# Kernel optimization log

Measured on AMD Instinct MI355X. Metric: run time of the kernel, lower is better.

## Reference

```python
import jax, jax.numpy as jnp
import numpy as np

B, L, D = 32, 128, 512
Qn = 16          # n_querys
N, P = 512, 64   # gathered groups x group size


def setup_inputs() -> dict:
    key = jax.random.key(0)
    ks = jax.random.split(key, 10)
    s = 0.02
    return {
        "patch": jax.random.normal(ks[0], (B, L, D), jnp.float32),
        "query": jax.random.normal(ks[1], (1, Qn, D), jnp.float32),
        "Wk": jax.random.normal(ks[2], (D, D), jnp.float32) * s,
        "bk": jnp.zeros((D,), jnp.float32),
        "Wv": jax.random.normal(ks[3], (D, D), jnp.float32) * s,
        "bv": jnp.zeros((D,), jnp.float32),
        "Wf": jax.random.normal(ks[4], (D, 1), jnp.float32) * s,
        "bf": jnp.zeros((1,), jnp.float32),
        "indices": jax.random.randint(ks[5], (N, P), 0, B * L),
        "pos_mask": jax.random.bernoulli(ks[6], 0.8, (N, P)),
    }


def reference(patch, query, Wk, bk, Wv, bv, Wf, bf, indices, pos_mask):
    # patch: [B,L,D]; query: [1,q,D]; indices: [N,P] into B*L; pos_mask: [N,P]
    b, l, d = patch.shape
    q = query.shape[1]
    scale = 1.0 / jnp.sqrt(jnp.asarray(d, patch.dtype))
    Q0 = query[0]                                   # [q,D]
    # Projections (proj_k/proj_v applied to [Q ; patch]); Q row identical across batch
    KQ = Q0 @ Wk + bk                               # [q,D]
    Kp = patch @ Wk + bk                            # [B,L,D]
    VQ = Q0 @ Wv + bv                               # [q,D]
    Vp = patch @ Wv + bv                            # [B,L,D]
    # attn scores: self-token column (same for every batch) + patch columns
    s_self = jnp.einsum('qd,qd->q', Q0, KQ) * scale            # [q]
    s_patch = jnp.einsum('qd,bld->blq', Q0, Kp) * scale        # [B,L,q]
    # gather groups of tokens by flat index
    g = s_patch.reshape(b * l, q)[indices]                     # [N,P,q]
    g = jnp.where(pos_mask[:, :, None], g, -jnp.inf)
    g = jnp.transpose(g, (0, 2, 1))                            # [N,q,P]
    scores = jnp.concatenate(
        [jnp.broadcast_to(s_self[None, :, None], (g.shape[0], q, 1)), g], axis=-1)
    w = jax.nn.softmax(scores, axis=-1)                        # [N,q,P+1]
    # gathered values (value of a token is independent of q in the original)
    Vg = Vp.reshape(b * l, d)[indices]                         # [N,P,D]
    Vg = jnp.where(pos_mask[:, :, None], Vg, 0.0)
    patch_token = w[:, :, 0:1] * VQ[None] \
        + jnp.einsum('nqp,npd->nqd', w[:, :, 1:], Vg)          # [N,q,D]
    # fusion attention pooling over the q query axis
    fw = jax.nn.softmax(jnp.einsum('nqd,do->nqo', patch_token, Wf) + bf, axis=1)
    return jnp.sum(patch_token * fw, axis=1)                   # [N,D]
```

## Files before the change

kernel.cpp:

```cpp
#include <hip/hip_runtime.h>
#include <hip/hip_bf16.h>
#include <math.h>

#define DD    512
#define QN    16
#define NTOK  4096
#define MEXT  4112
#define MPAD  4224
#define NGRP  512
#define PP    64
#define NB    640
#define SCALE 0.04419417382415922f

typedef __bf16 bf16x8 __attribute__((ext_vector_type(8)));
typedef float  f32x4  __attribute__((ext_vector_type(4)));

static __device__ __forceinline__ ushort f2bf(float f) {
    __hip_bfloat16 h = __float2bfloat16(f);
    return *reinterpret_cast<ushort*>(&h);
}
static __device__ __forceinline__ float2 bfp2f2(unsigned int v) {
    float2 r;
    r.x = __uint_as_float(v << 16);
    r.y = __uint_as_float(v & 0xffff0000u);
    return r;
}

__global__ __launch_bounds__(256) void pack_all(
    const float* __restrict__ patch, const float* __restrict__ query,
    const float* __restrict__ Wv, const float* __restrict__ Wk,
    const float* __restrict__ bk,
    ushort* __restrict__ Xb, ushort* __restrict__ Bb, float* __restrict__ c0)
{
    __shared__ float T[64][65];
    const int b = blockIdx.x;
    const int tid = threadIdx.x;
    if (b < 1056) {
        const int e0 = b * 2048 + tid * 8;
        const int row = e0 >> 9, c = e0 & 511;
        float v[8];
        if (row < NTOK) {
            const float4 a0 = *(const float4*)&patch[(size_t)row * DD + c];
            const float4 a1 = *(const float4*)&patch[(size_t)row * DD + c + 4];
            v[0]=a0.x; v[1]=a0.y; v[2]=a0.z; v[3]=a0.w;
            v[4]=a1.x; v[5]=a1.y; v[6]=a1.z; v[7]=a1.w;
        } else if (row < MEXT) {
            const float4 a0 = *(const float4*)&query[(size_t)(row - NTOK) * DD + c];
            const float4 a1 = *(const float4*)&query[(size_t)(row - NTOK) * DD + c + 4];
            v[0]=a0.x; v[1]=a0.y; v[2]=a0.z; v[3]=a0.w;
            v[4]=a1.x; v[5]=a1.y; v[6]=a1.z; v[7]=a1.w;
        } else {
#pragma unroll
            for (int j = 0; j < 8; ++j) v[j] = 0.f;
        }
        ushort o[8];
#pragma unroll
        for (int j = 0; j < 8; ++j) o[j] = f2bf(v[j]);
        *(uint4*)&Xb[e0] = *(const uint4*)o;
    } else if (b < 1120) {
        const int t = b - 1056;
        const int k0 = (t >> 3) * 64, n0 = (t & 7) * 64;
#pragma unroll
        for (int j = 0; j < 16; ++j) {
            const int idx = tid + j * 256;
            const int r = idx >> 6, c = idx & 63;
            T[r][c] = Wv[(size_t)(k0 + r) * DD + n0 + c];
        }
        __syncthreads();
#pragma unroll
        for (int j = 0; j < 16; ++j) {
            const int idx = tid + j * 256;
            const int r = idx >> 6, c = idx & 63;
            Bb[(size_t)(n0 + r) * DD + k0 + c] = f2bf(T[c][r]);
        }
    } else if (b < 1148) {
        const int e0 = (b - 1120) * 2048 + tid * 8;
        *(uint4*)&Bb[(size_t)528 * DD + e0] = make_uint4(0, 0, 0, 0);
    } else {
        const int wave = tid >> 6, lane = tid & 63;
        const int g = (b - 1148) * 4 + wave;
        if (g < DD) {
            const int e = g;
            float x[8];
#pragma unroll
            for (int j = 0; j < 8; ++j) x[j] = Wk[e * DD + j * 64 + lane];
            for (int q = 0; q < QN; ++q) {
                float s = 0.f;
#pragma unroll
                for (int j = 0; j < 8; ++j) s += x[j] * query[q * DD + j * 64 + lane];
#pragma unroll
                for (int off = 32; off > 0; off >>= 1) s += __shfl_down(s, off, 64);
                if (lane == 0) Bb[(size_t)(DD + q) * DD + e] = f2bf(s);
            }
        } else {
            const int q = g - DD;
            float s = 0.f;
#pragma unroll
            for (int j = 0; j < 8; ++j)
                s += bk[j * 64 + lane] * query[q * DD + j * 64 + lane];
#pragma unroll
            for (int off = 32; off > 0; off >>= 1) s += __shfl_down(s, off, 64);
            if (lane == 0) c0[q] = s;
        }
    }
}

__global__ __launch_bounds__(256) void k2_mfma(
    const ushort* __restrict__ Xb, const ushort* __restrict__ Bb,
    const float* __restrict__ bv, const float* __restrict__ c0,
    ushort* __restrict__ VpH, float* __restrict__ S)
{
    __shared__ __align__(16) ushort Xs[64][72];
    __shared__ __align__(16) ushort Bs[64][72];
    const int tid = threadIdx.x;
    const int rowBase = blockIdx.y * 64;
    const int colBase = blockIdx.x * 64;
    const int wave = tid >> 6, lane = tid & 63;
    const int wm = (wave >> 1) * 32, wn = (wave & 1) * 32;
    const int lr = lane & 15;
    const int quad = lane >> 4;

    f32x4 acc[2][2];
    const f32x4 zero = {0.f, 0.f, 0.f, 0.f};
#pragma unroll
    for (int i = 0; i < 2; ++i) { acc[i][0] = zero; acc[i][1] = zero; }

    for (int k0 = 0; k0 < DD; k0 += 64) {
#pragma unroll
        for (int i = 0; i < 2; ++i) {
            const int ch = tid + i * 256;
            const int r = ch >> 3, cc = (ch & 7) * 8;
            *(uint4*)&Xs[r][cc] = *(const uint4*)&Xb[(size_t)(rowBase + r) * DD + k0 + cc];
        }
#pragma unroll
        for (int i = 0; i < 2; ++i) {
            const int ch = tid + i * 256;
            const int r = ch >> 3, cc = (ch & 7) * 8;
            *(uint4*)&Bs[r][cc] = *(const uint4*)&Bb[(size_t)(colBase + r) * DD + k0 + cc];
        }
        __syncthreads();
#pragma unroll
        for (int kc = 0; kc < 2; ++kc) {
            bf16x8 af[2], bfr[2];
#pragma unroll
            for (int t = 0; t < 2; ++t)
                af[t] = *(const bf16x8*)&Xs[wm + t * 16 + lr][kc * 32 + quad * 8];
#pragma unroll
            for (int u = 0; u < 2; ++u)
                bfr[u] = *(const bf16x8*)&Bs[wn + u * 16 + lr][kc * 32 + quad * 8];
#pragma unroll
            for (int mt = 0; mt < 2; ++mt)
#pragma unroll
                for (int nt = 0; nt < 2; ++nt)
                    acc[mt][nt] = __builtin_amdgcn_mfma_f32_16x16x32_bf16(
                        af[mt], bfr[nt], acc[mt][nt], 0, 0, 0);
        }
        __syncthreads();
    }

#pragma unroll
    for (int nt = 0; nt < 2; ++nt) {
        const int col = colBase + wn + nt * 16 + lr;
        const bool isV = (col < DD);
        const bool isS = (col >= DD) && (col < DD + QN);
        const float badd = isV ? bv[col] : (isS ? c0[col - DD] : 0.f);
#pragma unroll
        for (int mt = 0; mt < 2; ++mt) {
#pragma unroll
            for (int r = 0; r < 4; ++r) {
                const int row = rowBase + wm + mt * 16 + quad * 4 + r;
                if (row < MEXT) {
                    const float v = acc[mt][nt][r];
                    if (isV)      VpH[(size_t)row * DD + col] = f2bf(v + badd);
                    else if (isS) S[row * QN + (col - DD)] = (v + badd) * SCALE;
                }
            }
        }
    }
}

__global__ __launch_bounds__(256) void k4_agg(
    const ushort* __restrict__ VpH,
    const float* __restrict__ S,
    const int* __restrict__ indices,
    const void* __restrict__ pmask,
    const float* __restrict__ Wf, const float* __restrict__ bf,
    float* __restrict__ out)
{
    __shared__ int   idxs[PP];
    __shared__ int   mval[PP];
    __shared__ int   cidx[PP + 4];
    __shared__ int   cp[PP + 4];
    __shared__ float scT[PP + 2][QN];
    __shared__ float red[QN][4];
    __shared__ float fwq[QN];
    __shared__ int   cntS;

    const int n = blockIdx.x;
    const int tid = threadIdx.x;

    const unsigned int* mw = (const unsigned int*)pmask;
    bool four = true;
#pragma unroll
    for (int i = 0; i < 16; ++i) {
        const unsigned int v = mw[i];
        four = four && (v == 0u || v == 1u || v == 0x3F800000u);
    }

    if (tid < PP) {
        idxs[tid] = indices[n * PP + tid];
        int mv;
        if (four) mv = (mw[n * PP + tid] != 0u);
        else      mv = (((const unsigned char*)pmask)[n * PP + tid] != 0);
        mval[tid] = mv;
        const bool a = (mv != 0);
        const unsigned long long m = __ballot(a);
        const int pos = __popcll(m & ((1ull << tid) - 1ull));
        if (a) { cidx[pos] = idxs[tid]; cp[pos] = tid; }
        if (tid == 0) cntS = (int)__popcll(m);
    }
    __syncthreads();

    for (int e = tid; e < QN * PP; e += 256) {
        const int p = e >> 4, q = e & 15;
        scT[p + 1][q] = mval[p] ? S[idxs[p] * QN + q] : -INFINITY;
    }
    if (tid < QN) scT[0][tid] = S[(NTOK + tid) * QN + tid];
    __syncthreads();

    if (tid < 4) { cidx[cntS + tid] = 0; cp[cntS + tid] = PP; }
    if (tid < QN) {
        const int q = tid;
        float m = -INFINITY;
        for (int j = 0; j <= PP; ++j) m = fmaxf(m, scT[j][q]);
        float s = 0.f;
        for (int j = 0; j <= PP; ++j) { const float e = __expf(scT[j][q] - m); scT[j][q] = e; s += e; }
        const float inv = 1.f / s;
        for (int j = 0; j <= PP; ++j) scT[j][q] *= inv;
        scT[PP + 1][q] = 0.f;
    }
    __syncthreads();

    const int cnt4 = (cntS + 3) & ~3;
    const int d0 = tid * 2;
    float pt[QN][2];
    {
        float2 vq[QN];
#pragma unroll
        for (int q = 0; q < QN; ++q)
            vq[q] = bfp2f2(*(const unsigned int*)&VpH[(size_t)(NTOK + q) * DD + d0]);
#pragma unroll
        for (int q = 0; q < QN; ++q) {
            const float w0 = scT[0][q];
            pt[q][0] = w0 * vq[q].x;
            pt[q][1] = w0 * vq[q].y;
        }
    }
    for (int j0 = 0; j0 < cnt4; j0 += 4) {
        float2 v[4]; int p[4];
#pragma unroll
        for (int pi = 0; pi < 4; ++pi) {
            v[pi] = bfp2f2(*(const unsigned int*)&VpH[(size_t)cidx[j0 + pi] * DD + d0]);
            p[pi] = cp[j0 + pi] + 1;
        }
#pragma unroll
        for (int pi = 0; pi < 4; ++pi) {
            const float4 wa = *(const float4*)&scT[p[pi]][0];
            const float4 wb = *(const float4*)&scT[p[pi]][4];
            const float4 wc = *(const float4*)&scT[p[pi]][8];
            const float4 wd = *(const float4*)&scT[p[pi]][12];
            const float vx = v[pi].x, vy = v[pi].y;
            pt[ 0][0] += wa.x*vx; pt[ 0][1] += wa.x*vy;
            pt[ 1][0] += wa.y*vx; pt[ 1][1] += wa.y*vy;
            pt[ 2][0] += wa.z*vx; pt[ 2][1] += wa.z*vy;
            pt[ 3][0] += wa.w*vx; pt[ 3][1] += wa.w*vy;
            pt[ 4][0] += wb.x*vx; pt[ 4][1] += wb.x*vy;
            pt[ 5][0] += wb.y*vx; pt[ 5][1] += wb.y*vy;
            pt[ 6][0] += wb.z*vx; pt[ 6][1] += wb.z*vy;
            pt[ 7][0] += wb.w*vx; pt[ 7][1] += wb.w*vy;
            pt[ 8][0] += wc.x*vx; pt[ 8][1] += wc.x*vy;
            pt[ 9][0] += wc.y*vx; pt[ 9][1] += wc.y*vy;
            pt[10][0] += wc.z*vx; pt[10][1] += wc.z*vy;
            pt[11][0] += wc.w*vx; pt[11][1] += wc.w*vy;
            pt[12][0] += wd.x*vx; pt[12][1] += wd.x*vy;
            pt[13][0] += wd.y*vx; pt[13][1] += wd.y*vy;
            pt[14][0] += wd.z*vx; pt[14][1] += wd.z*vy;
            pt[15][0] += wd.w*vx; pt[15][1] += wd.w*vy;
        }
    }

    const float wf0 = Wf[d0], wf1 = Wf[d0 + 1];
    const int wid = tid >> 6, lane = tid & 63;
#pragma unroll
    for (int q = 0; q < QN; ++q) {
        float s = pt[q][0] * wf0 + pt[q][1] * wf1;
#pragma unroll
        for (int off = 32; off > 0; off >>= 1) s += __shfl_down(s, off, 64);
        if (lane == 0) red[q][wid] = s;
    }
    __syncthreads();
    if (tid == 0) {
        float f[QN];
        float m = -INFINITY;
#pragma unroll
        for (int q = 0; q < QN; ++q) {
            f[q] = red[q][0] + red[q][1] + red[q][2] + red[q][3] + bf[0];
            m = fmaxf(m, f[q]);
        }
        float ssum = 0.f;
#pragma unroll
        for (int q = 0; q < QN; ++q) { f[q] = __expf(f[q] - m); ssum += f[q]; }
        const float inv = 1.f / ssum;
#pragma unroll
        for (int q = 0; q < QN; ++q) fwq[q] = f[q] * inv;
    }
    __syncthreads();

    float o0 = 0.f, o1 = 0.f;
#pragma unroll
    for (int q = 0; q < QN; ++q) {
        const float w = fwq[q];
        o0 += pt[q][0] * w;
        o1 += pt[q][1] * w;
    }
    *(float2*)&out[(size_t)n * DD + d0] = make_float2(o0, o1);
}

extern "C" void kernel_launch(void* const* d_in, const int* in_sizes, int n_in,
                              void* d_out, int out_size, void* d_ws, size_t ws_size,
                              hipStream_t stream)
{
    const float* patch   = (const float*)d_in[0];
    const float* query   = (const float*)d_in[1];
    const float* Wk      = (const float*)d_in[2];
    const float* bk      = (const float*)d_in[3];
    const float* Wv      = (const float*)d_in[4];
    const float* bv      = (const float*)d_in[5];
    const float* Wf      = (const float*)d_in[6];
    const float* bf      = (const float*)d_in[7];
    const int*   indices = (const int*)d_in[8];
    const void*  pmask   = d_in[9];
    float* out = (float*)d_out;

    ushort* VpH = (ushort*)d_ws;
    float*  S   = (float*)(VpH + (size_t)MEXT * DD);
    float*  c0  = S + (size_t)MEXT * QN;
    ushort* Xb  = (ushort*)(c0 + 16);
    ushort* Bb  = Xb + (size_t)MPAD * DD;

    pack_all<<<dim3(1280), dim3(256), 0, stream>>>(patch, query, Wv, Wk, bk, Xb, Bb, c0);
    k2_mfma <<<dim3(10, 66), dim3(256), 0, stream>>>(Xb, Bb, bv, c0, VpH, S);
    k4_agg  <<<dim3(NGRP), dim3(256), 0, stream>>>(VpH, S, indices, pmask, Wf, bf, out);
}
```

Before: 123.1 us.

## Fuse pack, GEMM and aggregation into one cooperative kernel with grid syncs

The three kernels (pack/convert, MFMA projection GEMM, gather-aggregate) become one persistent cooperative kernel of 512 blocks. Grid-wide syncs separate the stages, and shared memory is reused through one arena. The GEMM column tiles drop from 10 to 9, skipping the all-zero padded tile, and the zero-fill range shrinks to match. This removes two kernel launches and their inter-kernel gaps, at the cost of grid.sync overhead and fewer blocks for the pack and GEMM phases.

```diff
diff --git a/kernel.cpp b/kernel.cpp
--- a/kernel.cpp
+++ b/kernel.cpp
@@ -1,6 +1,9 @@
 #include <hip/hip_runtime.h>
 #include <hip/hip_bf16.h>
+#include <hip/hip_cooperative_groups.h>
 #include <math.h>
+
+namespace cg = cooperative_groups;
 
 #define DD    512
 #define QN    16
@@ -9,8 +12,10 @@
 #define MPAD  4224
 #define NGRP  512
 #define PP    64
-#define NB    640
+#define NB    576
 #define SCALE 0.04419417382415922f
+
+#define GRID  512
 
 typedef __bf16 bf16x8 __attribute__((ext_vector_type(8)));
 typedef float  f32x4  __attribute__((ext_vector_type(4)));
@@ -26,304 +31,302 @@
     return r;
 }
 
-__global__ __launch_bounds__(256) void pack_all(
+__global__ __launch_bounds__(256) void fused(
     const float* __restrict__ patch, const float* __restrict__ query,
-    const float* __restrict__ Wv, const float* __restrict__ Wk,
-    const float* __restrict__ bk,
-    ushort* __restrict__ Xb, ushort* __restrict__ Bb, float* __restrict__ c0)
+    const float* __restrict__ Wk,    const float* __restrict__ bk,
+    const float* __restrict__ Wv,    const float* __restrict__ bv,
+    const float* __restrict__ Wf,    const float* __restrict__ bf,
+    const int* __restrict__ indices, const void* __restrict__ pmask,
+    ushort* __restrict__ Xb, ushort* __restrict__ Bb, float* __restrict__ c0,
+    ushort* __restrict__ VpH, float* __restrict__ S, float* __restrict__ out)
 {
-    __shared__ float T[64][65];
-    const int b = blockIdx.x;
+    __shared__ __align__(16) unsigned char arena[18432];
+    cg::grid_group grid = cg::this_grid();
     const int tid = threadIdx.x;
-    if (b < 1056) {
-        const int e0 = b * 2048 + tid * 8;
-        const int row = e0 >> 9, c = e0 & 511;
-        float v[8];
-        if (row < NTOK) {
-            const float4 a0 = *(const float4*)&patch[(size_t)row * DD + c];
-            const float4 a1 = *(const float4*)&patch[(size_t)row * DD + c + 4];
-            v[0]=a0.x; v[1]=a0.y; v[2]=a0.z; v[3]=a0.w;
-            v[4]=a1.x; v[5]=a1.y; v[6]=a1.z; v[7]=a1.w;
-        } else if (row < MEXT) {
-            const float4 a0 = *(const float4*)&query[(size_t)(row - NTOK) * DD + c];
-            const float4 a1 = *(const float4*)&query[(size_t)(row - NTOK) * DD + c + 4];
-            v[0]=a0.x; v[1]=a0.y; v[2]=a0.z; v[3]=a0.w;
-            v[4]=a1.x; v[5]=a1.y; v[6]=a1.z; v[7]=a1.w;
-        } else {
-#pragma unroll
-            for (int j = 0; j < 8; ++j) v[j] = 0.f;
-        }
-        ushort o[8];
-#pragma unroll
-        for (int j = 0; j < 8; ++j) o[j] = f2bf(v[j]);
-        *(uint4*)&Xb[e0] = *(const uint4*)o;
-    } else if (b < 1120) {
-        const int t = b - 1056;
-        const int k0 = (t >> 3) * 64, n0 = (t & 7) * 64;
-#pragma unroll
-        for (int j = 0; j < 16; ++j) {
-            const int idx = tid + j * 256;
-            const int r = idx >> 6, c = idx & 63;
-            T[r][c] = Wv[(size_t)(k0 + r) * DD + n0 + c];
-        }
-        __syncthreads();
-#pragma unroll
-        for (int j = 0; j < 16; ++j) {
-            const int idx = tid + j * 256;
-            const int r = idx >> 6, c = idx & 63;
-            Bb[(size_t)(n0 + r) * DD + k0 + c] = f2bf(T[c][r]);
-        }
-    } else if (b < 1148) {
-        const int e0 = (b - 1120) * 2048 + tid * 8;
-        *(uint4*)&Bb[(size_t)528 * DD + e0] = make_uint4(0, 0, 0, 0);
-    } else {
+
+    {
+        float (*T)[65] = (float(*)[65])arena;
+        for (int b = blockIdx.x; b < 1264; b += GRID) {
+            if (b < 1056) {
+                const int e0 = b * 2048 + tid * 8;
+                const int row = e0 >> 9, c = e0 & 511;
+                float v[8];
+                if (row < NTOK) {
+                    const float4 a0 = *(const float4*)&patch[(size_t)row * DD + c];
+                    const float4 a1 = *(const float4*)&patch[(size_t)row * DD + c + 4];
+                    v[0]=a0.x; v[1]=a0.y; v[2]=a0.z; v[3]=a0.w;
+                    v[4]=a1.x; v[5]=a1.y; v[6]=a1.z; v[7]=a1.w;
+                } else if (row < MEXT) {
+                    const float4 a0 = *(const float4*)&query[(size_t)(row - NTOK) * DD + c];
+                    const float4 a1 = *(const float4*)&query[(size_t)(row - NTOK) * DD + c + 4];
+                    v[0]=a0.x; v[1]=a0.y; v[2]=a0.z; v[3]=a0.w;
+                    v[4]=a1.x; v[5]=a1.y; v[6]=a1.z; v[7]=a1.w;
+                } else {
+#pragma unroll
+                    for (int j = 0; j < 8; ++j) v[j] = 0.f;
+                }
+                ushort o[8];
+#pragma unroll
+                for (int j = 0; j < 8; ++j) o[j] = f2bf(v[j]);
+                *(uint4*)&Xb[e0] = *(const uint4*)o;
+            } else if (b < 1120) {
+                const int t = b - 1056;
+                const int k0 = (t >> 3) * 64, n0 = (t & 7) * 64;
+#pragma unroll
+                for (int j = 0; j < 16; ++j) {
+                    const int idx = tid + j * 256;
+                    const int r = idx >> 6, c = idx & 63;
+                    T[r][c] = Wv[(size_t)(k0 + r) * DD + n0 + c];
+                }
+                __syncthreads();
+#pragma unroll
+                for (int j = 0; j < 16; ++j) {
+                    const int idx = tid + j * 256;
+                    const int r = idx >> 6, c = idx & 63;
+                    Bb[(size_t)(n0 + r) * DD + k0 + c] = f2bf(T[c][r]);
+                }
+                __syncthreads();
+            } else if (b < 1132) {
+                const int e0 = (b - 1120) * 2048 + tid * 8;
+                *(uint4*)&Bb[(size_t)528 * DD + e0] = make_uint4(0, 0, 0, 0);
+            } else {
+                const int wave = tid >> 6, lane = tid & 63;
+                const int g = (b - 1132) * 4 + wave;
+                if (g < DD) {
+                    const int e = g;
+                    float x[8];
+#pragma unroll
+                    for (int j = 0; j < 8; ++j) x[j] = Wk[e * DD + j * 64 + lane];
+                    for (int q = 0; q < QN; ++q) {
+                        float s = 0.f;
+#pragma unroll
+                        for (int j = 0; j < 8; ++j) s += x[j] * query[q * DD + j * 64 + lane];
+#pragma unroll
+                        for (int off = 32; off > 0; off >>= 1) s += __shfl_down(s, off, 64);
+                        if (lane == 0) Bb[(size_t)(DD + q) * DD + e] = f2bf(s);
+                    }
+                } else {
+                    const int q = g - DD;
+                    float s = 0.f;
+#pragma unroll
+                    for (int j = 0; j < 8; ++j)
+                        s += bk[j * 64 + lane] * query[q * DD + j * 64 + lane];
+#pragma unroll
+                    for (int off = 32; off > 0; off >>= 1) s += __shfl_down(s, off, 64);
+                    if (lane == 0) c0[q] = s;
+                }
+            }
+        }
+    }
+
+    grid.sync();
+
+    {
+        ushort (*Xs)[72] = (ushort(*)[72])arena;
+        ushort (*Bs)[72] = (ushort(*)[72])(arena + 9216);
         const int wave = tid >> 6, lane = tid & 63;
-        const int g = (b - 1148) * 4 + wave;
-        if (g < DD) {
-            const int e = g;
-            float x[8];
-#pragma unroll
-            for (int j = 0; j < 8; ++j) x[j] = Wk[e * DD + j * 64 + lane];
+        const int wm = (wave >> 1) * 32, wn = (wave & 1) * 32;
+        const int lr = lane & 15;
+        const int quad = lane >> 4;
+
+        for (int tile = blockIdx.x; tile < 9 * 66; tile += GRID) {
+            const int rowBase = (tile / 9) * 64;
+            const int colBase = (tile % 9) * 64;
+
+            f32x4 acc[2][2];
+            const f32x4 zero = {0.f, 0.f, 0.f, 0.f};
+#pragma unroll
+            for (int i = 0; i < 2; ++i) { acc[i][0] = zero; acc[i][1] = zero; }
+
+            for (int k0 = 0; k0 < DD; k0 += 64) {
+#pragma unroll
+                for (int i = 0; i < 2; ++i) {
+                    const int ch = tid + i * 256;
+                    const int r = ch >> 3, cc = (ch & 7) * 8;
+                    *(uint4*)&Xs[r][cc] = *(const uint4*)&Xb[(size_t)(rowBase + r) * DD + k0 + cc];
+                    *(uint4*)&Bs[r][cc] = *(const uint4*)&Bb[(size_t)(colBase + r) * DD + k0 + cc];
+                }
+                __syncthreads();
+#pragma unroll
+                for (int kc = 0; kc < 2; ++kc) {
+                    bf16x8 af[2], bfr[2];
+#pragma unroll
+                    for (int t = 0; t < 2; ++t)
+                        af[t] = *(const bf16x8*)&Xs[wm + t * 16 + lr][kc * 32 + quad * 8];
+#pragma unroll
+                    for (int u = 0; u < 2; ++u)
+                        bfr[u] = *(const bf16x8*)&Bs[wn + u * 16 + lr][kc * 32 + quad * 8];
+#pragma unroll
+                    for (int mt = 0; mt < 2; ++mt)
+#pragma unroll
+                        for (int nt = 0; nt < 2; ++nt)
+                            acc[mt][nt] = __builtin_amdgcn_mfma_f32_16x16x32_bf16(
+                                af[mt], bfr[nt], acc[mt][nt], 0, 0, 0);
+                }
+                __syncthreads();
+            }
+
+#pragma unroll
+            for (int nt = 0; nt < 2; ++nt) {
+                const int col = colBase + wn + nt * 16 + lr;
+                const bool isV = (col < DD);
+                const bool isS = (col >= DD) && (col < DD + QN);
+                const float badd = isV ? bv[col] : (isS ? c0[col - DD] : 0.f);
+#pragma unroll
+                for (int mt = 0; mt < 2; ++mt) {
+#pragma unroll
+                    for (int r = 0; r < 4; ++r) {
+                        const int row = rowBase + wm + mt * 16 + quad * 4 + r;
+                        if (row < MEXT) {
+                            const float v = acc[mt][nt][r];
+                            if (isV)      VpH[(size_t)row * DD + col] = f2bf(v + badd);
+                            else if (isS) S[row * QN + (col - DD)] = (v + badd) * SCALE;
+                        }
+                    }
+                }
+            }
+        }
+    }
+
+    grid.sync();
+
+    {
+        int*   idxs = (int*)arena;
+        int*   mval = idxs + PP;
+        int*   cidx = mval + PP;
+        int*   cp   = cidx + (PP + 4);
+        float (*scT)[QN] = (float(*)[QN])(cp + (PP + 4));
+        float (*red)[4] = (float(*)[4])((float*)scT + 66 * QN);
+        float* fwq  = (float*)red + QN * 4;
+        int*   cntS = (int*)(fwq + QN);
+
+        const int n = blockIdx.x;
+        const unsigned int* mw = (const unsigned int*)pmask;
+        bool four = true;
+#pragma unroll
+        for (int i = 0; i < 16; ++i) {
+            const unsigned int v = mw[i];
+            four = four && (v == 0u || v == 1u || v == 0x3F800000u);
+        }
+
+        if (tid < PP) {
+            idxs[tid] = indices[n * PP + tid];
+            int mv;
+            if (four) mv = (mw[n * PP + tid] != 0u);
+            else      mv = (((const unsigned char*)pmask)[n * PP + tid] != 0);
+            mval[tid] = mv;
+            const bool a = (mv != 0);
+            const unsigned long long m = __ballot(a);
+            const int pos = __popcll(m & ((1ull << tid) - 1ull));
+            if (a) { cidx[pos] = idxs[tid]; cp[pos] = tid; }
+            if (tid == 0) *cntS = (int)__popcll(m);
+        }
+        __syncthreads();
+
+        for (int e = tid; e < QN * PP; e += 256) {
+            const int p = e >> 4, q = e & 15;
+            scT[p + 1][q] = mval[p] ? S[idxs[p] * QN + q] : -INFINITY;
+        }
+        if (tid < QN) scT[0][tid] = S[(NTOK + tid) * QN + tid];
+        __syncthreads();
+
+        if (tid < 4) { cidx[*cntS + tid] = 0; cp[*cntS + tid] = PP; }
+        if (tid < QN) {
+            const int q = tid;
+            float m = -INFINITY;
+            for (int j = 0; j <= PP; ++j) m = fmaxf(m, scT[j][q]);
+            float s = 0.f;
+            for (int j = 0; j <= PP; ++j) { const float e = __expf(scT[j][q] - m); scT[j][q] = e; s += e; }
+            const float inv = 1.f / s;
+            for (int j = 0; j <= PP; ++j) scT[j][q] *= inv;
+            scT[PP + 1][q] = 0.f;
+        }
+        __syncthreads();
+
+        const int cnt4 = (*cntS + 3) & ~3;
+        const int d0 = tid * 2;
+        float pt[QN][2];
+        {
+            float2 vq[QN];
+#pragma unroll
+            for (int q = 0; q < QN; ++q)
+                vq[q] = bfp2f2(*(const unsigned int*)&VpH[(size_t)(NTOK + q) * DD + d0]);
+#pragma unroll
             for (int q = 0; q < QN; ++q) {
-                float s = 0.f;
-#pragma unroll
-                for (int j = 0; j < 8; ++j) s += x[j] * query[q * DD + j * 64 + lane];
-#pragma unroll
-                for (int off = 32; off > 0; off >>= 1) s += __shfl_down(s, off, 64);
-                if (lane == 0) Bb[(size_t)(DD + q) * DD + e] = f2bf(s);
-            }
-        } else {
-            const int q = g - DD;
-            float s = 0.f;
-#pragma unroll
-            for (int j = 0; j < 8; ++j)
-                s += bk[j * 64 + lane] * query[q * DD + j * 64 + lane];
+                const float w0 = scT[0][q];
+                pt[q][0] = w0 * vq[q].x;
+                pt[q][1] = w0 * vq[q].y;
+            }
+        }
+        for (int j0 = 0; j0 < cnt4; j0 += 4) {
+            float2 v[4]; int p[4];
+#pragma unroll
+            for (int pi = 0; pi < 4; ++pi) {
+                v[pi] = bfp2f2(*(const unsigned int*)&VpH[(size_t)cidx[j0 + pi] * DD + d0]);
+                p[pi] = cp[j0 + pi] + 1;
+            }
+#pragma unroll
+            for (int pi = 0; pi < 4; ++pi) {
+                const float4 wa = *(const float4*)&scT[p[pi]][0];
+                const float4 wb = *(const float4*)&scT[p[pi]][4];
+                const float4 wc = *(const float4*)&scT[p[pi]][8];
+                const float4 wd = *(const float4*)&scT[p[pi]][12];
+                const float vx = v[pi].x, vy = v[pi].y;
+                pt[ 0][0] += wa.x*vx; pt[ 0][1] += wa.x*vy;
+                pt[ 1][0] += wa.y*vx; pt[ 1][1] += wa.y*vy;
+                pt[ 2][0] += wa.z*vx; pt[ 2][1] += wa.z*vy;
+                pt[ 3][0] += wa.w*vx; pt[ 3][1] += wa.w*vy;
+                pt[ 4][0] += wb.x*vx; pt[ 4][1] += wb.x*vy;
+                pt[ 5][0] += wb.y*vx; pt[ 5][1] += wb.y*vy;
+                pt[ 6][0] += wb.z*vx; pt[ 6][1] += wb.z*vy;
+                pt[ 7][0] += wb.w*vx; pt[ 7][1] += wb.w*vy;
+                pt[ 8][0] += wc.x*vx; pt[ 8][1] += wc.x*vy;
+                pt[ 9][0] += wc.y*vx; pt[ 9][1] += wc.y*vy;
+                pt[10][0] += wc.z*vx; pt[10][1] += wc.z*vy;
+                pt[11][0] += wc.w*vx; pt[11][1] += wc.w*vy;
+                pt[12][0] += wd.x*vx; pt[12][1] += wd.x*vy;
+                pt[13][0] += wd.y*vx; pt[13][1] += wd.y*vy;
+                pt[14][0] += wd.z*vx; pt[14][1] += wd.z*vy;
+                pt[15][0] += wd.w*vx; pt[15][1] += wd.w*vy;
+            }
+        }
+
+        const float wf0 = Wf[d0], wf1 = Wf[d0 + 1];
+        const int wid = tid >> 6, lane = tid & 63;
+#pragma unroll
+        for (int q = 0; q < QN; ++q) {
+            float s = pt[q][0] * wf0 + pt[q][1] * wf1;
 #pragma unroll
             for (int off = 32; off > 0; off >>= 1) s += __shfl_down(s, off, 64);
-            if (lane == 0) c0[q] = s;
-        }
+            if (lane == 0) red[q][wid] = s;
+        }
+        __syncthreads();
+        if (tid == 0) {
+            float f[QN];
+            float m = -INFINITY;
+#pragma unroll
+            for (int q = 0; q < QN; ++q) {
+                f[q] = red[q][0] + red[q][1] + red[q][2] + red[q][3] + bf[0];
+                m = fmaxf(m, f[q]);
+            }
+            float ssum = 0.f;
+#pragma unroll
+            for (int q = 0; q < QN; ++q) { f[q] = __expf(f[q] - m); ssum += f[q]; }
+            const float inv = 1.f / ssum;
+#pragma unroll
+            for (int q = 0; q < QN; ++q) fwq[q] = f[q] * inv;
+        }
+        __syncthreads();
+
+        float o0 = 0.f, o1 = 0.f;
+#pragma unroll
+        for (int q = 0; q < QN; ++q) {
+            const float w = fwq[q];
+            o0 += pt[q][0] * w;
+            o1 += pt[q][1] * w;
+        }
+        *(float2*)&out[(size_t)n * DD + d0] = make_float2(o0, o1);
     }
-}
-
-__global__ __launch_bounds__(256) void k2_mfma(
-    const ushort* __restrict__ Xb, const ushort* __restrict__ Bb,
-    const float* __restrict__ bv, const float* __restrict__ c0,
-    ushort* __restrict__ VpH, float* __restrict__ S)
-{
-    __shared__ __align__(16) ushort Xs[64][72];
-    __shared__ __align__(16) ushort Bs[64][72];
-    const int tid = threadIdx.x;
-    const int rowBase = blockIdx.y * 64;
-    const int colBase = blockIdx.x * 64;
-    const int wave = tid >> 6, lane = tid & 63;
-    const int wm = (wave >> 1) * 32, wn = (wave & 1) * 32;
-    const int lr = lane & 15;
-    const int quad = lane >> 4;
-
-    f32x4 acc[2][2];
-    const f32x4 zero = {0.f, 0.f, 0.f, 0.f};
-#pragma unroll
-    for (int i = 0; i < 2; ++i) { acc[i][0] = zero; acc[i][1] = zero; }
-
-    for (int k0 = 0; k0 < DD; k0 += 64) {
-#pragma unroll
-        for (int i = 0; i < 2; ++i) {
-            const int ch = tid + i * 256;
-            const int r = ch >> 3, cc = (ch & 7) * 8;
-            *(uint4*)&Xs[r][cc] = *(const uint4*)&Xb[(size_t)(rowBase + r) * DD + k0 + cc];
-        }
-#pragma unroll
-        for (int i = 0; i < 2; ++i) {
-            const int ch = tid + i * 256;
-            const int r = ch >> 3, cc = (ch & 7) * 8;
-            *(uint4*)&Bs[r][cc] = *(const uint4*)&Bb[(size_t)(colBase + r) * DD + k0 + cc];
-        }
-        __syncthreads();
-#pragma unroll
-        for (int kc = 0; kc < 2; ++kc) {
-            bf16x8 af[2], bfr[2];
-#pragma unroll
-            for (int t = 0; t < 2; ++t)
-                af[t] = *(const bf16x8*)&Xs[wm + t * 16 + lr][kc * 32 + quad * 8];
-#pragma unroll
-            for (int u = 0; u < 2; ++u)
-                bfr[u] = *(const bf16x8*)&Bs[wn + u * 16 + lr][kc * 32 + quad * 8];
-#pragma unroll
-            for (int mt = 0; mt < 2; ++mt)
-#pragma unroll
-                for (int nt = 0; nt < 2; ++nt)
-                    acc[mt][nt] = __builtin_amdgcn_mfma_f32_16x16x32_bf16(
-                        af[mt], bfr[nt], acc[mt][nt], 0, 0, 0);
-        }
-        __syncthreads();
-    }
-
-#pragma unroll
-    for (int nt = 0; nt < 2; ++nt) {
-        const int col = colBase + wn + nt * 16 + lr;
-        const bool isV = (col < DD);
-        const bool isS = (col >= DD) && (col < DD + QN);
-        const float badd = isV ? bv[col] : (isS ? c0[col - DD] : 0.f);
-#pragma unroll
-        for (int mt = 0; mt < 2; ++mt) {
-#pragma unroll
-            for (int r = 0; r < 4; ++r) {
-                const int row = rowBase + wm + mt * 16 + quad * 4 + r;
-                if (row < MEXT) {
-                    const float v = acc[mt][nt][r];
-                    if (isV)      VpH[(size_t)row * DD + col] = f2bf(v + badd);
-                    else if (isS) S[row * QN + (col - DD)] = (v + badd) * SCALE;
-                }
-            }
-        }
-    }
-}
-
-__global__ __launch_bounds__(256) void k4_agg(
-    const ushort* __restrict__ VpH,
-    const float* __restrict__ S,
-    const int* __restrict__ indices,
-    const void* __restrict__ pmask,
-    const float* __restrict__ Wf, const float* __restrict__ bf,
-    float* __restrict__ out)
-{
-    __shared__ int   idxs[PP];
-    __shared__ int   mval[PP];
-    __shared__ int   cidx[PP + 4];
-    __shared__ int   cp[PP + 4];
-    __shared__ float scT[PP + 2][QN];
-    __shared__ float red[QN][4];
-    __shared__ float fwq[QN];
-    __shared__ int   cntS;
-
-    const int n = blockIdx.x;
-    const int tid = threadIdx.x;
-
-    const unsigned int* mw = (const unsigned int*)pmask;
-    bool four = true;
-#pragma unroll
-    for (int i = 0; i < 16; ++i) {
-        const unsigned int v = mw[i];
-        four = four && (v == 0u || v == 1u || v == 0x3F800000u);
-    }
-
-    if (tid < PP) {
-        idxs[tid] = indices[n * PP + tid];
-        int mv;
-        if (four) mv = (mw[n * PP + tid] != 0u);
-        else      mv = (((const unsigned char*)pmask)[n * PP + tid] != 0);
-        mval[tid] = mv;
-        const bool a = (mv != 0);
-        const unsigned long long m = __ballot(a);
-        const int pos = __popcll(m & ((1ull << tid) - 1ull));
-        if (a) { cidx[pos] = idxs[tid]; cp[pos] = tid; }
-        if (tid == 0) cntS = (int)__popcll(m);
-    }
-    __syncthreads();
-
-    for (int e = tid; e < QN * PP; e += 256) {
-        const int p = e >> 4, q = e & 15;
-        scT[p + 1][q] = mval[p] ? S[idxs[p] * QN + q] : -INFINITY;
-    }
-    if (tid < QN) scT[0][tid] = S[(NTOK + tid) * QN + tid];
-    __syncthreads();
-
-    if (tid < 4) { cidx[cntS + tid] = 0; cp[cntS + tid] = PP; }
-    if (tid < QN) {
-        const int q = tid;
-        float m = -INFINITY;
-        for (int j = 0; j <= PP; ++j) m = fmaxf(m, scT[j][q]);
-        float s = 0.f;
-        for (int j = 0; j <= PP; ++j) { const float e = __expf(scT[j][q] - m); scT[j][q] = e; s += e; }
-        const float inv = 1.f / s;
-        for (int j = 0; j <= PP; ++j) scT[j][q] *= inv;
-        scT[PP + 1][q] = 0.f;
-    }
-    __syncthreads();
-
-    const int cnt4 = (cntS + 3) & ~3;
-    const int d0 = tid * 2;
-    float pt[QN][2];
-    {
-        float2 vq[QN];
-#pragma unroll
-        for (int q = 0; q < QN; ++q)
-            vq[q] = bfp2f2(*(const unsigned int*)&VpH[(size_t)(NTOK + q) * DD + d0]);
-#pragma unroll
-        for (int q = 0; q < QN; ++q) {
-            const float w0 = scT[0][q];
-            pt[q][0] = w0 * vq[q].x;
-            pt[q][1] = w0 * vq[q].y;
-        }
-    }
-    for (int j0 = 0; j0 < cnt4; j0 += 4) {
-        float2 v[4]; int p[4];
-#pragma unroll
-        for (int pi = 0; pi < 4; ++pi) {
-            v[pi] = bfp2f2(*(const unsigned int*)&VpH[(size_t)cidx[j0 + pi] * DD + d0]);
-            p[pi] = cp[j0 + pi] + 1;
-        }
-#pragma unroll
-        for (int pi = 0; pi < 4; ++pi) {
-            const float4 wa = *(const float4*)&scT[p[pi]][0];
-            const float4 wb = *(const float4*)&scT[p[pi]][4];
-            const float4 wc = *(const float4*)&scT[p[pi]][8];
-            const float4 wd = *(const float4*)&scT[p[pi]][12];
-            const float vx = v[pi].x, vy = v[pi].y;
-            pt[ 0][0] += wa.x*vx; pt[ 0][1] += wa.x*vy;
-            pt[ 1][0] += wa.y*vx; pt[ 1][1] += wa.y*vy;
-            pt[ 2][0] += wa.z*vx; pt[ 2][1] += wa.z*vy;
-            pt[ 3][0] += wa.w*vx; pt[ 3][1] += wa.w*vy;
-            pt[ 4][0] += wb.x*vx; pt[ 4][1] += wb.x*vy;
-            pt[ 5][0] += wb.y*vx; pt[ 5][1] += wb.y*vy;
-            pt[ 6][0] += wb.z*vx; pt[ 6][1] += wb.z*vy;
-            pt[ 7][0] += wb.w*vx; pt[ 7][1] += wb.w*vy;
-            pt[ 8][0] += wc.x*vx; pt[ 8][1] += wc.x*vy;
-            pt[ 9][0] += wc.y*vx; pt[ 9][1] += wc.y*vy;
-            pt[10][0] += wc.z*vx; pt[10][1] += wc.z*vy;
-            pt[11][0] += wc.w*vx; pt[11][1] += wc.w*vy;
-            pt[12][0] += wd.x*vx; pt[12][1] += wd.x*vy;
-            pt[13][0] += wd.y*vx; pt[13][1] += wd.y*vy;
-            pt[14][0] += wd.z*vx; pt[14][1] += wd.z*vy;
-            pt[15][0] += wd.w*vx; pt[15][1] += wd.w*vy;
-        }
-    }
-
-    const float wf0 = Wf[d0], wf1 = Wf[d0 + 1];
-    const int wid = tid >> 6, lane = tid & 63;
-#pragma unroll
-    for (int q = 0; q < QN; ++q) {
-        float s = pt[q][0] * wf0 + pt[q][1] * wf1;
-#pragma unroll
-        for (int off = 32; off > 0; off >>= 1) s += __shfl_down(s, off, 64);
-        if (lane == 0) red[q][wid] = s;
-    }
-    __syncthreads();
-    if (tid == 0) {
-        float f[QN];
-        float m = -INFINITY;
-#pragma unroll
-        for (int q = 0; q < QN; ++q) {
-            f[q] = red[q][0] + red[q][1] + red[q][2] + red[q][3] + bf[0];
-            m = fmaxf(m, f[q]);
-        }
-        float ssum = 0.f;
-#pragma unroll
-        for (int q = 0; q < QN; ++q) { f[q] = __expf(f[q] - m); ssum += f[q]; }
-        const float inv = 1.f / ssum;
-#pragma unroll
-        for (int q = 0; q < QN; ++q) fwq[q] = f[q] * inv;
-    }
-    __syncthreads();
-
-    float o0 = 0.f, o1 = 0.f;
-#pragma unroll
-    for (int q = 0; q < QN; ++q) {
-        const float w = fwq[q];
-        o0 += pt[q][0] * w;
-        o1 += pt[q][1] * w;
-    }
-    *(float2*)&out[(size_t)n * DD + d0] = make_float2(o0, o1);
 }
 
 extern "C" void kernel_launch(void* const* d_in, const int* in_sizes, int n_in,
@@ -348,7 +351,12 @@
     ushort* Xb  = (ushort*)(c0 + 16);
     ushort* Bb  = Xb + (size_t)MPAD * DD;
 
-    pack_all<<<dim3(1280), dim3(256), 0, stream>>>(patch, query, Wv, Wk, bk, Xb, Bb, c0);
-    k2_mfma <<<dim3(10, 66), dim3(256), 0, stream>>>(Xb, Bb, bv, c0, VpH, S);
-    k4_agg  <<<dim3(NGRP), dim3(256), 0, stream>>>(VpH, S, indices, pmask, Wf, bf, out);
+    void* args[] = {
+        (void*)&patch, (void*)&query, (void*)&Wk, (void*)&bk,
+        (void*)&Wv, (void*)&bv, (void*)&Wf, (void*)&bf,
+        (void*)&indices, (void*)&pmask,
+        (void*)&Xb, (void*)&Bb, (void*)&c0, (void*)&VpH, (void*)&S, (void*)&out
+    };
+    hipLaunchCooperativeKernel((const void*)fused, dim3(GRID), dim3(256),
+                               args, 0, stream);
 }
```

Result: slower. 260.7 us (+111.8%).
